# Optimization experiments

Measured on AMD Instinct MI355X. Metric: run time of the kernel, lower is better.

## Reference

```python
import jax, jax.numpy as jnp
import numpy as np

N_HEADS = 8  # SD UNet default for hidden_size=1280
ADAPTER_SCALE = 1.0  # self.scale in SSRAttnProcessor


def setup_inputs() -> dict:
    key = jax.random.key(0)
    ks = jax.random.split(key, 7)
    B, S, D = 16, 4096, 1280
    T, C = 77, 768
    return {
        "hidden_states": jax.random.normal(ks[0], (B, S, D), jnp.float32),
        "encoder_hidden_states": jax.random.normal(ks[1], (B, T, C), jnp.float32),
        "w_q": jax.random.normal(ks[2], (D, D), jnp.float32) * (D ** -0.5),
        "w_k_ssr": jax.random.normal(ks[3], (D, C), jnp.float32) * (C ** -0.5),
        "w_v_ssr": jax.random.normal(ks[4], (D, C), jnp.float32) * (C ** -0.5),
        "w_out": jax.random.normal(ks[5], (D, D), jnp.float32) * (D ** -0.5),
        "b_out": jnp.zeros((D,), jnp.float32),
    }


def reference(hidden_states, encoder_hidden_states, w_q, w_k_ssr, w_v_ssr, w_out, b_out):
    B, S, D = hidden_states.shape
    T = encoder_hidden_states.shape[1]
    H = N_HEADS
    d = D // H
    # projections (torch Linear: x @ W^T)
    q = jnp.einsum('bsc,dc->bsd', hidden_states, w_q)
    k = jnp.einsum('btc,dc->btd', encoder_hidden_states, w_k_ssr)
    v = jnp.einsum('btc,dc->btd', encoder_hidden_states, w_v_ssr)
    # head split: [B, H, S, d]
    q = q.reshape(B, S, H, d).transpose(0, 2, 1, 3)
    k = k.reshape(B, T, H, d).transpose(0, 2, 1, 3)
    v = v.reshape(B, T, H, d).transpose(0, 2, 1, 3)
    # attn.get_attention_scores: softmax(Q K^T * d^-0.5)
    scores = jnp.einsum('bhsd,bhtd->bhst', q, k) * (d ** -0.5)
    probs = jax.nn.softmax(scores, axis=-1)
    out = jnp.einsum('bhst,bhtd->bhsd', probs, v)
    out = out.transpose(0, 2, 1, 3).reshape(B, S, D)
    out = ADAPTER_SCALE * out
    # to_out[0] linear (+ identity dropout); residual_connection=False, rescale=1
    out = jnp.einsum('bsd,ed->bse', out, w_out) + b_out
    return out
```

## Files before the change

kernel.cpp:

```cpp
#include <hip/hip_runtime.h>
#include <hip/hip_bf16.h>

typedef __bf16 bf16x8 __attribute__((ext_vector_type(8)));
typedef short  short8 __attribute__((ext_vector_type(8)));
typedef float  f32x4  __attribute__((ext_vector_type(4)));

__device__ __forceinline__ short f2bs(float f) {
  return __builtin_bit_cast(short, __float2bfloat16(f));
}

__device__ __forceinline__ bf16x8 ldfrag(const short* p) {
  return *reinterpret_cast<const bf16x8*>(p);
}

__device__ __forceinline__ void gl2lds16(const short* g, short* lds_base) {
  __builtin_amdgcn_global_load_lds(
      (const __attribute__((address_space(1))) unsigned int*)g,
      (__attribute__((address_space(3))) unsigned int*)lds_base, 16, 0, 0);
}

__global__ __launch_bounds__(256) void cast8_f32_bf16(const float* __restrict__ in,
                                                      short* __restrict__ out, long n) {
  long i = ((long)blockIdx.x * 256 + threadIdx.x) * 8;
  if (i < n) {
    float4 a = *reinterpret_cast<const float4*>(in + i);
    float4 b = *reinterpret_cast<const float4*>(in + i + 4);
    short8 v;
    v[0] = f2bs(a.x); v[1] = f2bs(a.y); v[2] = f2bs(a.z); v[3] = f2bs(a.w);
    v[4] = f2bs(b.x); v[5] = f2bs(b.y); v[6] = f2bs(b.z); v[7] = f2bs(b.w);
    *reinterpret_cast<short8*>(out + i) = v;
  }
}

template <typename OT, bool BIAS>
__global__ __launch_bounds__(256)
void gemm_fast(const short* __restrict__ A, const short* __restrict__ B,
               const float* __restrict__ bias, OT* __restrict__ C,
               int M, int N, int K) {
  __shared__ short As[128 * 32];
  __shared__ short Bs[128 * 32];

  const int tid  = threadIdx.x;
  const int wave = tid >> 6, lane = tid & 63;
  const int quad = lane >> 4, l16 = lane & 15;
  const int wy = wave >> 1, wx = wave & 1;
  const size_t row0 = (size_t)blockIdx.y * 128, col0 = (size_t)blockIdx.x * 128;

  const int srow = lane >> 2;
  const int scol = (lane & 3) * 8;

  const short* Ab0 = A + (row0 + wave * 32 + srow) * (size_t)K + scol;
  const short* Ab1 = Ab0 + (size_t)16 * K;
  const short* Bb0 = B + (col0 + wave * 32 + srow) * (size_t)K + scol;
  const short* Bb1 = Bb0 + (size_t)16 * K;
  short* const Al0 = &As[(wave * 32) * 32];
  short* const Al1 = &As[(wave * 32 + 16) * 32];
  short* const Bl0 = &Bs[(wave * 32) * 32];
  short* const Bl1 = &Bs[(wave * 32 + 16) * 32];

  f32x4 acc[4][4] = {};

  for (int k0 = 0; k0 < K; k0 += 32) {
    gl2lds16(Ab0 + k0, Al0);
    gl2lds16(Ab1 + k0, Al1);
    gl2lds16(Bb0 + k0, Bl0);
    gl2lds16(Bb1 + k0, Bl1);
    __syncthreads();

    bf16x8 af[4], bv[4];
#pragma unroll
    for (int i = 0; i < 4; i++) af[i] = ldfrag(&As[(wy * 64 + i * 16 + l16) * 32 + quad * 8]);
#pragma unroll
    for (int i = 0; i < 4; i++) bv[i] = ldfrag(&Bs[(wx * 64 + i * 16 + l16) * 32 + quad * 8]);
#pragma unroll
    for (int mi = 0; mi < 4; mi++)
#pragma unroll
      for (int ni = 0; ni < 4; ni++)
        acc[mi][ni] = __builtin_amdgcn_mfma_f32_16x16x32_bf16(af[mi], bv[ni], acc[mi][ni], 0, 0, 0);
    __syncthreads();
  }

#pragma unroll
  for (int mi = 0; mi < 4; mi++) {
#pragma unroll
    for (int r = 0; r < 4; r++) {
      const size_t row = row0 + wy * 64 + mi * 16 + quad * 4 + r;
#pragma unroll
      for (int ni = 0; ni < 4; ni++) {
        const size_t col = col0 + wx * 64 + ni * 16 + l16;
        float v = acc[mi][ni][r];
        if constexpr (BIAS) v += bias[col];
        if constexpr (sizeof(OT) == 4)
          C[row * N + col] = v;
        else
          C[row * N + col] = f2bs(v);
      }
    }
  }
}

__global__ __launch_bounds__(256)
void gemm_small(const float* __restrict__ A, const short* __restrict__ B,
                short* __restrict__ C, int M, int N, int K) {
  __shared__ short As[128][40];
  __shared__ short Bs[128][40];

  const int tid  = threadIdx.x;
  const int wave = tid >> 6, lane = tid & 63;
  const int quad = lane >> 4, l16 = lane & 15;
  const int wy = wave >> 1, wx = wave & 1;
  const int row0 = blockIdx.y * 128, col0 = blockIdx.x * 128;
  const int sr = tid >> 2;
  const int sc = (tid & 3) * 8;

  f32x4 acc[4][4] = {};

  for (int k0 = 0; k0 < K; k0 += 32) {
    for (int p = 0; p < 128; p += 64) {
      const int r  = sr + p;
      const int gm = row0 + r;
      short8 va = {0, 0, 0, 0, 0, 0, 0, 0};
      if (gm < M) {
        const float* ap = A + (size_t)gm * K + k0 + sc;
        float4 x = *reinterpret_cast<const float4*>(ap);
        float4 y = *reinterpret_cast<const float4*>(ap + 4);
        va[0] = f2bs(x.x); va[1] = f2bs(x.y); va[2] = f2bs(x.z); va[3] = f2bs(x.w);
        va[4] = f2bs(y.x); va[5] = f2bs(y.y); va[6] = f2bs(y.z); va[7] = f2bs(y.w);
      }
      *reinterpret_cast<short8*>(&As[r][sc]) = va;
      *reinterpret_cast<short8*>(&Bs[r][sc]) =
          *reinterpret_cast<const short8*>(B + (size_t)(col0 + r) * K + k0 + sc);
    }
    __syncthreads();

    bf16x8 af[4], bv[4];
#pragma unroll
    for (int i = 0; i < 4; i++) af[i] = ldfrag(&As[wy * 64 + i * 16 + l16][quad * 8]);
#pragma unroll
    for (int i = 0; i < 4; i++) bv[i] = ldfrag(&Bs[wx * 64 + i * 16 + l16][quad * 8]);
#pragma unroll
    for (int mi = 0; mi < 4; mi++)
#pragma unroll
      for (int ni = 0; ni < 4; ni++)
        acc[mi][ni] = __builtin_amdgcn_mfma_f32_16x16x32_bf16(af[mi], bv[ni], acc[mi][ni], 0, 0, 0);
    __syncthreads();
  }

#pragma unroll
  for (int mi = 0; mi < 4; mi++) {
#pragma unroll
    for (int r = 0; r < 4; r++) {
      const int row = row0 + wy * 64 + mi * 16 + quad * 4 + r;
      if (row >= M) continue;
#pragma unroll
      for (int ni = 0; ni < 4; ni++) {
        const int col = col0 + wx * 64 + ni * 16 + l16;
        C[(size_t)row * N + col] = f2bs(acc[mi][ni][r]);
      }
    }
  }
}

__global__ __launch_bounds__(256)
void attn_kernel(const short* __restrict__ Kp, const short* __restrict__ Vp,
                 const short* __restrict__ Qin, short* __restrict__ Oout) {
  __shared__ short Vt[160][104];
  __shared__ short Pl[4][16][104];

  const int tid  = threadIdx.x;
  const int b = blockIdx.z, h = blockIdx.y, s0 = blockIdx.x * 64;
  const int wave = tid >> 6, lane = tid & 63;
  const int quad = lane >> 4, l16 = lane & 15;

  for (int idx = tid; idx < 77 * 160; idx += 256) {
    int t = idx / 160, i = idx - t * 160;
    Vt[i][t] = Vp[((size_t)(b * 77 + t)) * 1280 + h * 160 + i];
  }
  for (int idx = tid; idx < 160 * 19; idx += 256) {
    int i = idx / 19, t = 77 + (idx - i * 19);
    Vt[i][t] = 0;
  }
  __syncthreads();

  const short* Qg = Qin + ((size_t)b * 4096 + s0 + wave * 16 + l16) * 1280 + h * 160;
  bf16x8 qf[5];
#pragma unroll
  for (int kc = 0; kc < 5; kc++) qf[kc] = ldfrag(Qg + kc * 32 + quad * 8);

  f32x4 scv[5];
#pragma unroll
  for (int nt = 0; nt < 5; nt++) {
    f32x4 s = {};
    const short* Kg = Kp + ((size_t)(b * 77) + nt * 16 + l16) * 1280 + h * 160;
#pragma unroll
    for (int kc = 0; kc < 5; kc++) {
      bf16x8 kf = ldfrag(Kg + kc * 32 + quad * 8);
      s = __builtin_amdgcn_mfma_f32_16x16x32_bf16(qf[kc], kf, s, 0, 0, 0);
    }
    scv[nt] = s;
  }

  const float scale = 0.07905694150420949f;
#pragma unroll
  for (int r = 0; r < 4; r++) {
    float v[5];
    float m = -1e30f;
#pragma unroll
    for (int nt = 0; nt < 5; nt++) {
      v[nt] = scv[nt][r];
      if (nt * 16 + l16 < 77) m = fmaxf(m, v[nt]);
    }
#pragma unroll
    for (int off = 1; off < 16; off <<= 1) m = fmaxf(m, __shfl_xor(m, off));
    float sum = 0.f, p[5];
#pragma unroll
    for (int nt = 0; nt < 5; nt++) {
      p[nt] = (nt * 16 + l16 < 77) ? __expf((v[nt] - m) * scale) : 0.f;
      sum += p[nt];
    }
#pragma unroll
    for (int off = 1; off < 16; off <<= 1) sum += __shfl_xor(sum, off);
    const float inv = 1.f / sum;
    const int q = quad * 4 + r;
#pragma unroll
    for (int nt = 0; nt < 5; nt++) Pl[wave][q][nt * 16 + l16] = f2bs(p[nt] * inv);
    Pl[wave][q][80 + l16] = 0;
  }
  __syncthreads();

  bf16x8 pf[3];
#pragma unroll
  for (int kc = 0; kc < 3; kc++) pf[kc] = ldfrag(&Pl[wave][l16][kc * 32 + quad * 8]);

  short* Og = Oout + ((size_t)b * 4096 + s0 + wave * 16) * 1280 + h * 160;
#pragma unroll
  for (int nt = 0; nt < 10; nt++) {
    f32x4 o = {};
#pragma unroll
    for (int kc = 0; kc < 3; kc++) {
      bf16x8 vf = ldfrag(&Vt[nt * 16 + l16][kc * 32 + quad * 8]);
      o = __builtin_amdgcn_mfma_f32_16x16x32_bf16(pf[kc], vf, o, 0, 0, 0);
    }
#pragma unroll
    for (int r = 0; r < 4; r++) {
      const int q = quad * 4 + r;
      Og[(size_t)q * 1280 + nt * 16 + l16] = f2bs(o[r]);
    }
  }
}

extern "C" void kernel_launch(void* const* d_in, const int* in_sizes, int n_in,
                              void* d_out, int out_size, void* d_ws, size_t ws_size,
                              hipStream_t stream) {
  const float* hs  = (const float*)d_in[0];
  const float* enc = (const float*)d_in[1];
  const float* wq  = (const float*)d_in[2];
  const float* wk  = (const float*)d_in[3];
  const float* wv  = (const float*)d_in[4];
  const float* wo  = (const float*)d_in[5];
  const float* bo  = (const float*)d_in[6];
  float* out = (float*)d_out;

  char* ws = (char*)d_ws;
  short* wq_bf = (short*)(ws + 0);
  short* wk_bf = (short*)(ws + 3276800);
  short* wv_bf = (short*)(ws + 5242880);
  short* wo_bf = (short*)(ws + 7208960);
  short* Kp    = (short*)(ws + 10485760);
  short* Vp    = (short*)(ws + 13660160);
  short* Xbf   = (short*)(ws + 16834560);
  if (ws_size < (size_t)184606720) return;

  short* Qb = (short*)d_out;

  cast8_f32_bf16<<<800, 256, 0, stream>>>(wq, wq_bf, 1638400);
  cast8_f32_bf16<<<480, 256, 0, stream>>>(wk, wk_bf, 983040);
  cast8_f32_bf16<<<480, 256, 0, stream>>>(wv, wv_bf, 983040);
  cast8_f32_bf16<<<800, 256, 0, stream>>>(wo, wo_bf, 1638400);
  cast8_f32_bf16<<<40960, 256, 0, stream>>>(hs, Xbf, 83886080);

  dim3 g_kv(10, 10);
  gemm_small<<<g_kv, 256, 0, stream>>>(enc, wk_bf, Kp, 1232, 1280, 768);
  gemm_small<<<g_kv, 256, 0, stream>>>(enc, wv_bf, Vp, 1232, 1280, 768);

  dim3 g_q(10, 512);
  gemm_fast<short, false><<<g_q, 256, 0, stream>>>(Xbf, wq_bf, nullptr, Qb, 65536, 1280, 1280);

  dim3 g_a(64, 8, 16);
  attn_kernel<<<g_a, 256, 0, stream>>>(Kp, Vp, Qb, Xbf);

  gemm_fast<float, true><<<g_q, 256, 0, stream>>>(Xbf, wo_bf, bo, out, 65536, 1280, 1280);
}
```

Measured before the change: 1.533 ms.

## Replace bf16 GEMMs with 256x256-tile triple-buffered pipelined kernel

The two large projection GEMMs now use a new kernel with 256x256 output tiles and 512 threads. K tiles are loaded straight into LDS through a three-stage buffer, so the next tiles are fetched while MFMAs run on the current one, with one barrier per iteration. It also adds an XOR swizzle on the LDS layout to avoid bank conflicts, a grid swizzle of block indices for L2 reuse, and s_setprio around the MFMA block. In exchange, each wave holds twice as many accumulators and LDS use grows to 96KB per block, which may limit occupancy to a single block per CU.

```diff
diff --git a/kernel.cpp b/kernel.cpp
--- a/kernel.cpp
+++ b/kernel.cpp
@@ -33,61 +33,94 @@
 }
 
 template <typename OT, bool BIAS>
-__global__ __launch_bounds__(256)
-void gemm_fast(const short* __restrict__ A, const short* __restrict__ B,
+__global__ __launch_bounds__(512, 2)
+void gemm_pipe(const short* __restrict__ A, const short* __restrict__ B,
                const float* __restrict__ bias, OT* __restrict__ C,
                int M, int N, int K) {
-  __shared__ short As[128 * 32];
-  __shared__ short Bs[128 * 32];
+  __shared__ __align__(16) short As[3][8192];
+  __shared__ __align__(16) short Bs[3][8192];
 
   const int tid  = threadIdx.x;
   const int wave = tid >> 6, lane = tid & 63;
   const int quad = lane >> 4, l16 = lane & 15;
-  const int wy = wave >> 1, wx = wave & 1;
-  const size_t row0 = (size_t)blockIdx.y * 128, col0 = (size_t)blockIdx.x * 128;
-
-  const int srow = lane >> 2;
-  const int scol = (lane & 3) * 8;
-
-  const short* Ab0 = A + (row0 + wave * 32 + srow) * (size_t)K + scol;
-  const short* Ab1 = Ab0 + (size_t)16 * K;
-  const short* Bb0 = B + (col0 + wave * 32 + srow) * (size_t)K + scol;
-  const short* Bb1 = Bb0 + (size_t)16 * K;
-  short* const Al0 = &As[(wave * 32) * 32];
-  short* const Al1 = &As[(wave * 32 + 16) * 32];
-  short* const Bl0 = &Bs[(wave * 32) * 32];
-  short* const Bl1 = &Bs[(wave * 32 + 16) * 32];
-
-  f32x4 acc[4][4] = {};
-
-  for (int k0 = 0; k0 < K; k0 += 32) {
-    gl2lds16(Ab0 + k0, Al0);
-    gl2lds16(Ab1 + k0, Al1);
-    gl2lds16(Bb0 + k0, Bl0);
-    gl2lds16(Bb1 + k0, Bl1);
-    __syncthreads();
-
-    bf16x8 af[4], bv[4];
-#pragma unroll
-    for (int i = 0; i < 4; i++) af[i] = ldfrag(&As[(wy * 64 + i * 16 + l16) * 32 + quad * 8]);
-#pragma unroll
-    for (int i = 0; i < 4; i++) bv[i] = ldfrag(&Bs[(wx * 64 + i * 16 + l16) * 32 + quad * 8]);
-#pragma unroll
-    for (int mi = 0; mi < 4; mi++)
+  const int wm = wave >> 2, wn = wave & 3;
+
+  const int nwg = gridDim.x;
+  int swz = blockIdx.x;
+  if ((nwg & 7) == 0) {
+    const int per = nwg >> 3;
+    swz = (swz & 7) * per + (swz >> 3);
+  }
+  const int ntx = N >> 8;
+  const int bx = swz % ntx, by = swz / ntx;
+  const size_t row0 = (size_t)by << 8, col0 = (size_t)bx << 8;
+
+  const int sr = lane >> 2;
+  const int sq = (lane & 3) ^ (sr & 3);
+  const short* Ag0 = A + (row0 + wave * 32 +      sr) * (size_t)K + sq * 8;
+  const short* Ag1 = A + (row0 + wave * 32 + 16 + sr) * (size_t)K + sq * 8;
+  const short* Bg0 = B + (col0 + wave * 32 +      sr) * (size_t)K + sq * 8;
+  const short* Bg1 = B + (col0 + wave * 32 + 16 + sr) * (size_t)K + sq * 8;
+  const int lds0 = wave * 1024;
+
+  const int aBase = (wm * 128 + l16) * 32 + ((quad ^ (l16 & 3)) * 8);
+  const int bBase = (wn * 64  + l16) * 32 + ((quad ^ (l16 & 3)) * 8);
+
+  f32x4 acc[8][4] = {};
+  const int NT = K >> 5;
+
+  auto stage = [&](int buf, int t) {
+    const int ko = t << 5;
+    gl2lds16(Ag0 + ko, &As[buf][lds0]);
+    gl2lds16(Ag1 + ko, &As[buf][lds0 + 512]);
+    gl2lds16(Bg0 + ko, &Bs[buf][lds0]);
+    gl2lds16(Bg1 + ko, &Bs[buf][lds0 + 512]);
+  };
+
+  auto compute = [&](int buf) {
+    bf16x8 af[8], bv[4];
+#pragma unroll
+    for (int i = 0; i < 8; i++) af[i] = ldfrag(&As[buf][aBase + i * 512]);
+#pragma unroll
+    for (int i = 0; i < 4; i++) bv[i] = ldfrag(&Bs[buf][bBase + i * 512]);
+    __builtin_amdgcn_s_setprio(1);
+#pragma unroll
+    for (int mi = 0; mi < 8; mi++)
 #pragma unroll
       for (int ni = 0; ni < 4; ni++)
         acc[mi][ni] = __builtin_amdgcn_mfma_f32_16x16x32_bf16(af[mi], bv[ni], acc[mi][ni], 0, 0, 0);
-    __syncthreads();
-  }
-
-#pragma unroll
-  for (int mi = 0; mi < 4; mi++) {
+    __builtin_amdgcn_s_setprio(0);
+  };
+
+  stage(0, 0);
+  stage(1, 1);
+  asm volatile("s_waitcnt vmcnt(4)" ::: "memory");
+  __builtin_amdgcn_s_barrier();
+  asm volatile("" ::: "memory");
+
+  for (int t = 0; t < NT; ++t) {
+    const int cur = t % 3;
+    if (t + 2 < NT) {
+      stage((t + 2) % 3, t + 2);
+      compute(cur);
+      asm volatile("s_waitcnt vmcnt(4)" ::: "memory");
+    } else {
+      compute(cur);
+      asm volatile("s_waitcnt vmcnt(0)" ::: "memory");
+    }
+    __builtin_amdgcn_s_barrier();
+    asm volatile("" ::: "memory");
+    __builtin_amdgcn_sched_barrier(0);
+  }
+
+#pragma unroll
+  for (int mi = 0; mi < 8; mi++) {
 #pragma unroll
     for (int r = 0; r < 4; r++) {
-      const size_t row = row0 + wy * 64 + mi * 16 + quad * 4 + r;
+      const size_t row = row0 + wm * 128 + mi * 16 + quad * 4 + r;
 #pragma unroll
       for (int ni = 0; ni < 4; ni++) {
-        const size_t col = col0 + wx * 64 + ni * 16 + l16;
+        const size_t col = col0 + wn * 64 + ni * 16 + l16;
         float v = acc[mi][ni][r];
         if constexpr (BIAS) v += bias[col];
         if constexpr (sizeof(OT) == 4)
@@ -283,11 +316,10 @@
   gemm_small<<<g_kv, 256, 0, stream>>>(enc, wk_bf, Kp, 1232, 1280, 768);
   gemm_small<<<g_kv, 256, 0, stream>>>(enc, wv_bf, Vp, 1232, 1280, 768);
 
-  dim3 g_q(10, 512);
-  gemm_fast<short, false><<<g_q, 256, 0, stream>>>(Xbf, wq_bf, nullptr, Qb, 65536, 1280, 1280);
+  gemm_pipe<short, false><<<1280, 512, 0, stream>>>(Xbf, wq_bf, nullptr, Qb, 65536, 1280, 1280);
 
   dim3 g_a(64, 8, 16);
   attn_kernel<<<g_a, 256, 0, stream>>>(Kp, Vp, Qb, Xbf);
 
-  gemm_fast<float, true><<<g_q, 256, 0, stream>>>(Xbf, wo_bf, bo, out, 65536, 1280, 1280);
-}
+  gemm_pipe<float, true><<<1280, 512, 0, stream>>>(Xbf, wo_bf, bo, out, 65536, 1280, 1280);
+}
```

New measurement: 3.026 ms. 1.97x slower.
